# Kernel tuning notes

Measured on AMD Instinct MI355X. Metric: run time of the kernel, lower is better.

Reference implementation:

```python
import jax, jax.numpy as jnp
import numpy as np

B, N, C, H, L, M, V, NC = 8, 2048, 512, 8, 8, 128, 32000, 2
HD = C // H          # head dim = 64
HID = 4 * C          # MLP hidden = 2048
SCALE = HD ** -0.5
LN_EPS = 1e-5
FEAT_EPS = 1e-6


def _orth_matrix(d, m, rng):
    # gaussian_orthogonal_random_matrix: stack QR blocks of d x d
    blocks = []
    n_full, m_rem = divmod(m, d)
    for _ in range(n_full):
        Q, _ = np.linalg.qr(rng.standard_normal((d, d)))
        blocks.append(Q)
    if m_rem > 0:
        Q, _ = np.linalg.qr(rng.standard_normal((d, d)))
        blocks.append(Q[:, :m_rem])
    return np.concatenate(blocks, axis=1)


def setup_inputs() -> dict:
    key = jax.random.key(0)
    ks = jax.random.split(key, 32)
    rng = np.random.default_rng(0)

    def w(i, shape, s=0.02):
        return jax.random.normal(ks[i], shape, jnp.float32) * s

    proj = jnp.asarray(
        np.stack([np.stack([_orth_matrix(HD, M, rng) for _ in range(H)]) for _ in range(L)]),
        jnp.float32)  # [L, H, HD, M]

    inp = {
        "input_ids": jax.random.randint(ks[0], (B, N), 0, V),
        "attention_mask": jnp.ones((B, N), jnp.int32),
        "tok_emb": w(1, (V, C)),
        "cls": w(2, (1, 1, C)),
        "pos": w(3, (N + 1, C)),
        "ln1_g": jnp.ones((L, C), jnp.float32),
        "ln1_b": jnp.zeros((L, C), jnp.float32),
        "qW": w(4, (L, C, C)), "qb": jnp.zeros((L, C), jnp.float32),
        "kW": w(5, (L, C, C)), "kb": jnp.zeros((L, C), jnp.float32),
        "vW": w(6, (L, C, C)), "vb": jnp.zeros((L, C), jnp.float32),
        "oW": w(7, (L, C, C)), "ob": jnp.zeros((L, C), jnp.float32),
        "proj": proj,
        "ln2_g": jnp.ones((L, C), jnp.float32),
        "ln2_b": jnp.zeros((L, C), jnp.float32),
        "fc1W": w(8, (L, C, HID)), "fc1b": jnp.zeros((L, HID), jnp.float32),
        "fc2W": w(9, (L, HID, C)), "fc2b": jnp.zeros((L, C), jnp.float32),
        "lnf_g": jnp.ones((C,), jnp.float32),
        "lnf_b": jnp.zeros((C,), jnp.float32),
        "headW": w(10, (C, NC)),
        "headb": jnp.zeros((NC,), jnp.float32),
    }
    return inp


def _ln(x, g, b):
    mu = jnp.mean(x, axis=-1, keepdims=True)
    var = jnp.mean((x - mu) ** 2, axis=-1, keepdims=True)
    return (x - mu) * jax.lax.rsqrt(var + LN_EPS) * g + b


def _softmax_feature(x, p):
    # x: [B,Nt,H,HD], p: [H,HD,M]
    xw = jnp.einsum('bnhd,hdm->bnhm', x, p)
    x_sq = 0.5 * jnp.sum(x * x, axis=-1, keepdims=True)
    mx = jnp.max(xw, axis=-1, keepdims=True)
    return jnp.exp(xw - mx) * jnp.exp(mx - x_sq) + FEAT_EPS


def reference(input_ids, attention_mask, tok_emb, cls, pos, ln1_g, ln1_b,
              qW, qb, kW, kb, vW, vb, oW, ob, proj, ln2_g, ln2_b,
              fc1W, fc1b, fc2W, fc2b, lnf_g, lnf_b, headW, headb):
    x = tok_emb[input_ids]                                   # [B,N,C]
    x = jnp.concatenate([jnp.broadcast_to(cls, (B, 1, C)), x], axis=1)  # [B,Nt,C]
    x = x + pos[None]
    mask = jnp.concatenate(
        [jnp.ones((B, 1), x.dtype), attention_mask.astype(x.dtype)], axis=1)  # [B,Nt]
    mfeat = mask[:, :, None, None]

    Nt = N + 1
    for i in range(L):
        # Performer attention (FAVOR+)
        y = _ln(x, ln1_g[i], ln1_b[i])
        q = (y @ qW[i] + qb[i]).reshape(B, Nt, H, HD) * SCALE
        k = (y @ kW[i] + kb[i]).reshape(B, Nt, H, HD) * mfeat
        v = (y @ vW[i] + vb[i]).reshape(B, Nt, H, HD) * mfeat
        qf = _softmax_feature(q, proj[i])                    # [B,Nt,H,M]
        kf = _softmax_feature(k, proj[i])
        kv = jnp.einsum('bnhm,bnhd->bhmd', kf, v)            # [B,H,M,HD]
        ksum = jnp.sum(kf, axis=1)                           # [B,H,M]
        denom = jnp.maximum(jnp.einsum('bnhm,bhm->bhn', qf, ksum), 1e-6)[..., None]
        ctx = jnp.einsum('bnhm,bhmd->bhnd', qf, kv) / denom  # [B,H,Nt,HD]
        out = ctx.transpose(0, 2, 1, 3).reshape(B, Nt, C)
        x = x + (out @ oW[i] + ob[i])
        # MLP (exact GELU, as nn.GELU default)
        y = _ln(x, ln2_g[i], ln2_b[i])
        h = jax.nn.gelu(y @ fc1W[i] + fc1b[i], approximate=False)
        x = x + (h @ fc2W[i] + fc2b[i])

    x = _ln(x, lnf_g, lnf_b)
    return x[:, 0] @ headW + headb                           # [B,NC]
```

## Files before the change

### kernel.cpp

```cpp
#include <hip/hip_runtime.h>
#include <cmath>
#include <cstdint>
#include <cstddef>

#define B_ 8
#define N_ 2048
#define NT 2049
#define NP 2080
#define C_ 512
#define H_ 8
#define HD_ 64
#define L_ 8
#define M_ 128
#define HID_ 2048
#define NC_ 2
#define BNT (B_*NT)
#define RP (B_*NP)
#define SCALE_ 0.125f
#define LN_EPS_ 1e-5f
#define FEAT_EPS_ 1e-6f

#define MODE_GELU  2
#define MODE_RESID 3

typedef unsigned short u16;
typedef unsigned short u16x8 __attribute__((ext_vector_type(8)));
typedef short frag __attribute__((ext_vector_type(8)));
typedef float f32x4 __attribute__((ext_vector_type(4)));

constexpr size_t F_X    = 0;
constexpr size_t F_KVP  = F_X   + (size_t)RP*512;
constexpr size_t F_KSP  = F_KVP + (size_t)4*64*8192;
constexpr size_t F_KV   = F_KSP + (size_t)4*64*128;
constexpr size_t F_KS   = F_KV  + (size_t)64*M_*HD_;
constexpr size_t F_QKVB = F_KS  + (size_t)64*M_;
constexpr size_t F_END  = F_QKVB + 1536;
constexpr size_t S_BASE = 2 * F_END;
constexpr size_t S_Y    = S_BASE;
constexpr size_t S_V    = S_Y  + (size_t)RP*512;
constexpr size_t S_KF   = S_V  + (size_t)RP*512;
constexpr size_t S_QF   = S_KF + (size_t)RP*1024;
constexpr size_t S_WQKV = S_QF + (size_t)RP*1024;
constexpr size_t S_WO   = S_WQKV + (size_t)1536*512;
constexpr size_t S_WF1  = S_WO   + (size_t)512*512;
constexpr size_t S_WF2  = S_WF1  + (size_t)2048*512;
constexpr size_t S_PT   = S_WF2  + (size_t)512*2048;
constexpr size_t S_END  = S_PT   + (size_t)8*128*64;
constexpr size_t WS_BYTES = S_END * 2;

__device__ __forceinline__ float wave_reduce(float v) {
#pragma unroll
  for (int off = 32; off > 0; off >>= 1) v += __shfl_down(v, off, 64);
  return v;
}
__device__ __forceinline__ float b2f(u16 u) {
  union { float f; uint32_t i; } v; v.i = ((uint32_t)u) << 16; return v.f;
}
__device__ __forceinline__ u16 f2b(float f) {
  union { float f; uint32_t i; } v; v.f = f;
  uint32_t r = v.i + 0x7FFF + ((v.i >> 16) & 1);
  return (u16)(r >> 16);
}
__device__ __forceinline__ void gstage(const u16* g, u16* lds_base, int lane) {
#if __has_builtin(__builtin_amdgcn_global_load_lds)
  __builtin_amdgcn_global_load_lds((const __attribute__((address_space(1))) void*)g,
      (__attribute__((address_space(3))) void*)lds_base, 16, 0, 0);
#else
  *(u16x8*)(lds_base + lane * 8) = *(const u16x8*)g;
#endif
}
__device__ __forceinline__ void xcd_swz(int& bx, int& by) {
  int gx = gridDim.x;
  int nwg = gx * gridDim.y;
  int hw = blockIdx.x + blockIdx.y * gx;
  if (nwg & 7) { bx = blockIdx.x; by = blockIdx.y; return; }
  int cpx = nwg >> 3;
  int swz = (hw & 7) * cpx + (hw >> 3);
  bx = swz % gx; by = swz / gx;
}

__global__ __launch_bounds__(256) void embed_k(const int* __restrict__ ids,
    const float* __restrict__ tok, const float* __restrict__ cls,
    const float* __restrict__ pos, float* __restrict__ X) {
  int row = blockIdx.x;
  int b = row / NT, n = row - b * NT;
  int t = threadIdx.x;
  const float* src = (n == 0) ? cls : tok + (size_t)ids[b * N_ + n - 1] * C_;
  size_t rp = (size_t)b * NP + n;
  X[rp * C_ + t]       = src[t]       + pos[(size_t)n * C_ + t];
  X[rp * C_ + t + 256] = src[t + 256] + pos[(size_t)n * C_ + t + 256];
}

__global__ __launch_bounds__(256) void wconv_k(
    const float* __restrict__ qW, const float* __restrict__ kW,
    const float* __restrict__ vW, const float* __restrict__ oW,
    const float* __restrict__ f1W, const float* __restrict__ f2W,
    const float* __restrict__ projL,
    const float* __restrict__ qb, const float* __restrict__ kb,
    const float* __restrict__ vb,
    u16* __restrict__ Wqkv, u16* __restrict__ Wo,
    u16* __restrict__ Wf1, u16* __restrict__ Wf2,
    u16* __restrict__ PT, float* __restrict__ QKVB) {
  __shared__ float tile[32][33];
  int bid = blockIdx.x, t = threadIdx.x;
  if (bid >= 3104) {
    int i = (bid - 3104) * 256 + t;
    QKVB[i] = (i < 512) ? qb[i] : (i < 1024) ? kb[i - 512] : vb[i - 1024];
    return;
  }
  if (bid >= 3072) {
    int base = (bid - 3072) * 2048 + t * 8;
#pragma unroll
    for (int j = 0; j < 8; ++j) {
      int idx = base + j;
      int h = idx >> 13, rem = idx & 8191, m = rem >> 6, d = rem & 63;
      PT[idx] = f2b(projL[(size_t)h * 8192 + d * 128 + m]);
    }
    return;
  }
  int ti = t >> 5, tj = t & 31;
  const float* src; u16* dst; int k0, n0, ldn, ldk, scol;
  if (bid < 768) {
    int tk = bid & 15, tn = bid >> 4;
    k0 = tk * 32; n0 = tn * 32;
    int sel = n0 >> 9; scol = n0 & 511;
    src = (sel == 0) ? qW : (sel == 1) ? kW : vW;
    ldn = 512; dst = Wqkv; ldk = 512;
  } else if (bid < 1024) {
    int b2 = bid - 768;
    int tk = b2 & 15, tn = b2 >> 4;
    k0 = tk * 32; n0 = tn * 32; scol = n0;
    src = oW; ldn = 512; dst = Wo; ldk = 512;
  } else if (bid < 2048) {
    int b2 = bid - 1024;
    int tk = b2 & 15, tn = b2 >> 4;
    k0 = tk * 32; n0 = tn * 32; scol = n0;
    src = f1W; ldn = 2048; dst = Wf1; ldk = 512;
  } else {
    int b2 = bid - 2048;
    int tk = b2 & 63, tn = b2 >> 6;
    k0 = tk * 32; n0 = tn * 32; scol = n0;
    src = f2W; ldn = 512; dst = Wf2; ldk = 2048;
  }
  const float* sp = src + (size_t)k0 * ldn + scol;
  u16* dp = dst + (size_t)n0 * ldk + k0;
#pragma unroll
  for (int p = 0; p < 4; ++p)
    tile[ti + p * 8][tj] = sp[(size_t)(ti + p * 8) * ldn + tj];
  __syncthreads();
#pragma unroll
  for (int p = 0; p < 4; ++p)
    dp[(size_t)(ti + p * 8) * ldk + tj] = f2b(tile[tj][ti + p * 8]);
}

__global__ __launch_bounds__(256) void ln_bf_k(const float* __restrict__ X,
    const float* __restrict__ g, const float* __restrict__ b,
    u16* __restrict__ Y) {
  int w = threadIdx.x >> 6, lane = threadIdx.x & 63;
  int row = blockIdx.x * 4 + w;
  const float* xr = X + (size_t)row * C_;
  float v[8];
  *(float4*)&v[0] = *(const float4*)(xr + lane * 8);
  *(float4*)&v[4] = *(const float4*)(xr + lane * 8 + 4);
  float s = 0.f;
#pragma unroll
  for (int j = 0; j < 8; ++j) s += v[j];
  s = wave_reduce(s);
  float mu = __shfl(s, 0, 64) * (1.0f / C_);
  float sq = 0.f;
#pragma unroll
  for (int j = 0; j < 8; ++j) { float d = v[j] - mu; sq = fmaf(d, d, sq); }
  sq = wave_reduce(sq);
  float rs = rsqrtf(__shfl(sq, 0, 64) * (1.0f / C_) + LN_EPS_);
  float gv[8], bv[8];
  *(float4*)&gv[0] = *(const float4*)(g + lane * 8);
  *(float4*)&gv[4] = *(const float4*)(g + lane * 8 + 4);
  *(float4*)&bv[0] = *(const float4*)(b + lane * 8);
  *(float4*)&bv[4] = *(const float4*)(b + lane * 8 + 4);
  u16x8 o;
#pragma unroll
  for (int j = 0; j < 8; ++j) o[j] = f2b((v[j] - mu) * rs * gv[j] + bv[j]);
  *(u16x8*)(Y + (size_t)row * C_ + lane * 8) = o;
}

__global__ __launch_bounds__(256) void gemm_bf_k(
    const u16* __restrict__ A, int lda,
    const u16* __restrict__ Wt,
    const float* __restrict__ bias,
    float* __restrict__ outF, u16* __restrict__ outB,
    int ldc, int Kdim, int mode) {
  __shared__ __align__(16) u16 As[128 * 64];
  __shared__ __align__(16) u16 Bs[128 * 64];
  const int t = threadIdx.x, w = t >> 6, l = t & 63;
  int bx, by; xcd_swz(bx, by);
  const int row0 = by * 128, col0 = bx * 128;
  const int wm = w & 1, wn = w >> 1;
  const int lm = l & 15, lkb = l >> 4;
  const int lr = l >> 3, lc = l & 7;
  const int kch = (lc ^ lr) * 8;
  const u16* Ag = A  + (size_t)(row0 + lr) * lda  + kch;
  const u16* Bg = Wt + (size_t)(col0 + lr) * Kdim + kch;
  const int sx = lm & 7;
  f32x4 acc[4][4] = {};
  for (int k0 = 0; k0 < Kdim; k0 += 64) {
    __syncthreads();
#pragma unroll
    for (int j = 0; j < 4; ++j) {
      int c8 = w * 4 + j;
      gstage(Ag + (size_t)c8 * 8 * lda  + k0, &As[c8 * 512], l);
      gstage(Bg + (size_t)c8 * 8 * Kdim + k0, &Bs[c8 * 512], l);
    }
    __syncthreads();
#pragma unroll
    for (int ks = 0; ks < 2; ++ks) {
      frag af[4], bf4[4];
#pragma unroll
      for (int i = 0; i < 4; ++i)
        af[i] = *(const frag*)&As[(wm * 64 + i * 16 + lm) * 64 + (((ks * 4 + lkb) ^ sx) * 8)];
#pragma unroll
      for (int j = 0; j < 4; ++j)
        bf4[j] = *(const frag*)&Bs[(wn * 64 + j * 16 + lm) * 64 + (((ks * 4 + lkb) ^ sx) * 8)];
#pragma unroll
      for (int i = 0; i < 4; ++i)
#pragma unroll
        for (int j = 0; j < 4; ++j)
          acc[i][j] = __builtin_amdgcn_mfma_f32_16x16x32_bf16(af[i], bf4[j], acc[i][j], 0, 0, 0);
    }
  }
#pragma unroll
  for (int i = 0; i < 4; ++i) {
#pragma unroll
    for (int r = 0; r < 4; ++r) {
      int grow = row0 + wm * 64 + i * 16 + lkb * 4 + r;
      if (mode == MODE_RESID) {
        float* orow = outF + (size_t)grow * ldc + col0;
#pragma unroll
        for (int j = 0; j < 4; ++j) {
          int gc = wn * 64 + j * 16 + lm;
          orow[gc] += acc[i][j][r] + bias[col0 + gc];
        }
      } else {
        u16* orow = outB + (size_t)grow * ldc + col0;
#pragma unroll
        for (int j = 0; j < 4; ++j) {
          int gc = wn * 64 + j * 16 + lm;
          float v = acc[i][j][r] + bias[col0 + gc];
          float u = v * (1.5957691216f + 0.0713548162f * v * v);
          v = v / (1.f + __expf(-u));
          orow[gc] = f2b(v);
        }
      }
    }
  }
}

__global__ __launch_bounds__(256) void gemm_bf64_k(
    const u16* __restrict__ A, int lda,
    const u16* __restrict__ Wt,
    const float* __restrict__ bias,
    float* __restrict__ outF, u16* __restrict__ outB,
    int ldc, int Kdim, int mode) {
  __shared__ __align__(16) u16 As[64 * 64];
  __shared__ __align__(16) u16 Bs[128 * 64];
  const int t = threadIdx.x, w = t >> 6, l = t & 63;
  int bx, by; xcd_swz(bx, by);
  const int row0 = by * 64, col0 = bx * 128;
  const int wm = w & 1, wn = w >> 1;
  const int lm = l & 15, lkb = l >> 4;
  const int lr = l >> 3, lc = l & 7;
  const int kch = (lc ^ lr) * 8;
  const u16* Ag = A  + (size_t)(row0 + lr) * lda  + kch;
  const u16* Bg = Wt + (size_t)(col0 + lr) * Kdim + kch;
  const int sx = lm & 7;
  f32x4 acc[2][4] = {};
  for (int k0 = 0; k0 < Kdim; k0 += 64) {
    __syncthreads();
#pragma unroll
    for (int q = 0; q < 2; ++q) {
      int c8 = w * 2 + q;
      gstage(Ag + (size_t)c8 * 8 * lda + k0, &As[c8 * 512], l);
    }
#pragma unroll
    for (int q = 0; q < 4; ++q) {
      int c8 = w * 4 + q;
      gstage(Bg + (size_t)c8 * 8 * Kdim + k0, &Bs[c8 * 512], l);
    }
    __syncthreads();
#pragma unroll
    for (int ks = 0; ks < 2; ++ks) {
      frag af[2], bf4[4];
#pragma unroll
      for (int i = 0; i < 2; ++i)
        af[i] = *(const frag*)&As[(wm * 32 + i * 16 + lm) * 64 + (((ks * 4 + lkb) ^ sx) * 8)];
#pragma unroll
      for (int j = 0; j < 4; ++j)
        bf4[j] = *(const frag*)&Bs[(wn * 64 + j * 16 + lm) * 64 + (((ks * 4 + lkb) ^ sx) * 8)];
#pragma unroll
      for (int i = 0; i < 2; ++i)
#pragma unroll
        for (int j = 0; j < 4; ++j)
          acc[i][j] = __builtin_amdgcn_mfma_f32_16x16x32_bf16(af[i], bf4[j], acc[i][j], 0, 0, 0);
    }
  }
#pragma unroll
  for (int i = 0; i < 2; ++i) {
#pragma unroll
    for (int r = 0; r < 4; ++r) {
      int grow = row0 + wm * 32 + i * 16 + lkb * 4 + r;
      if (mode == MODE_RESID) {
        float* orow = outF + (size_t)grow * ldc + col0;
#pragma unroll
        for (int j = 0; j < 4; ++j) {
          int gc = wn * 64 + j * 16 + lm;
          orow[gc] += acc[i][j][r] + bias[col0 + gc];
        }
      } else {
        u16* orow = outB + (size_t)grow * ldc + col0;
#pragma unroll
        for (int j = 0; j < 4; ++j) {
          int gc = wn * 64 + j * 16 + lm;
          float v = acc[i][j][r] + bias[col0 + gc];
          float u = v * (1.5957691216f + 0.0713548162f * v * v);
          v = v / (1.f + __expf(-u));
          orow[gc] = f2b(v);
        }
      }
    }
  }
}

__global__ __launch_bounds__(256) void gemmqkv_k(
    const u16* __restrict__ A,
    const u16* __restrict__ Wt,
    const float* __restrict__ bias,
    u16* __restrict__ Vout,
    u16* __restrict__ QF, u16* __restrict__ KF,
    const u16* __restrict__ PT,
    const int* __restrict__ attn) {
  __shared__ __align__(16) u16 As[128 * 64];
  __shared__ __align__(16) u16 Bs[128 * 64];
  __shared__ __align__(16) u16 ptb[128 * 64];
  __shared__ float sxe[128][2];
  const int t = threadIdx.x, w = t >> 6, l = t & 63;
  int bx, by; xcd_swz(bx, by);
  const int cx = bx;
  const int row0 = by * 128, col0 = cx * 128;
  const int wm = w & 1, wn = w >> 1;
  const int lm = l & 15, lkb = l >> 4;
  const int lr = l >> 3, lc = l & 7;
  const int kch = (lc ^ lr) * 8;
  const u16* Ag = A  + (size_t)(row0 + lr) * 512 + kch;
  const u16* Bg = Wt + (size_t)(col0 + lr) * 512 + kch;
  const int sx = lm & 7;
  f32x4 acc[4][4] = {};
  for (int k0 = 0; k0 < 512; k0 += 64) {
    __syncthreads();
#pragma unroll
    for (int j = 0; j < 4; ++j) {
      int c8 = w * 4 + j;
      gstage(Ag + (size_t)c8 * 8 * 512 + k0, &As[c8 * 512], l);
      gstage(Bg + (size_t)c8 * 8 * 512 + k0, &Bs[c8 * 512], l);
    }
    __syncthreads();
#pragma unroll
    for (int ks = 0; ks < 2; ++ks) {
      frag af[4], bf4[4];
#pragma unroll
      for (int i = 0; i < 4; ++i)
        af[i] = *(const frag*)&As[(wm * 64 + i * 16 + lm) * 64 + (((ks * 4 + lkb) ^ sx) * 8)];
#pragma unroll
      for (int j = 0; j < 4; ++j)
        bf4[j] = *(const frag*)&Bs[(wn * 64 + j * 16 + lm) * 64 + (((ks * 4 + lkb) ^ sx) * 8)];
#pragma unroll
      for (int i = 0; i < 4; ++i)
#pragma unroll
        for (int j = 0; j < 4; ++j)
          acc[i][j] = __builtin_amdgcn_mfma_f32_16x16x32_bf16(af[i], bf4[j], acc[i][j], 0, 0, 0);
    }
  }
  if (cx >= 8) {
    int c0v = col0 - 1024;
#pragma unroll
    for (int i = 0; i < 4; ++i) {
#pragma unroll
      for (int r = 0; r < 4; ++r) {
        int grow = row0 + wm * 64 + i * 16 + lkb * 4 + r;
        int bb = grow / NP, nn = grow - bb * NP;
        float mrow = (nn == 0) ? 1.f : ((nn < NT) ? (float)attn[bb * N_ + nn - 1] : 0.f);
        u16* orow = Vout + (size_t)grow * 512 + c0v;
#pragma unroll
        for (int j = 0; j < 4; ++j) {
          int gc = wn * 64 + j * 16 + lm;
          orow[gc] = f2b((acc[i][j][r] + bias[col0 + gc]) * mrow);
        }
      }
    }
    return;
  }
  const bool isq = (cx < 4);
  const int hbase = (isq ? cx : cx - 4) * 2;
  __syncthreads();
  {
    u16* qt = wn ? Bs : As;
#pragma unroll
    for (int i = 0; i < 4; ++i) {
#pragma unroll
      for (int r = 0; r < 4; ++r) {
        int rl = wm * 64 + i * 16 + lkb * 4 + r;
        float mrow;
        if (isq) mrow = SCALE_;
        else {
          int grow = row0 + rl;
          int bb = grow / NP, nn = grow - bb * NP;
          mrow = (nn == 0) ? 1.f : ((nn < NT) ? (float)attn[bb * N_ + nn - 1] : 0.f);
        }
#pragma unroll
        for (int j = 0; j < 4; ++j) {
          int gcc = j * 16 + lm;
          float v = (acc[i][j][r] + bias[col0 + wn * 64 + gcc]) * mrow;
          qt[rl * 64 + (((gcc >> 3) ^ (rl & 7)) * 8) + (gcc & 7)] = f2b(v);
        }
      }
    }
  }
  {
    const u16* Pg = PT + (size_t)hbase * 8192 + (size_t)lr * 64 + kch;
#pragma unroll
    for (int q = 0; q < 4; ++q) {
      int c8 = w * 4 + q;
      gstage(Pg + (size_t)c8 * 8 * 64, &ptb[c8 * 512], l);
    }
  }
  __syncthreads();
  {
    int rowi = t >> 1, hf = t & 1;
    const u16* qq = hf ? Bs : As;
    float s = 0.f;
#pragma unroll
    for (int c = 0; c < 8; ++c) {
      const u16* p = &qq[rowi * 64 + ((c ^ (rowi & 7)) * 8)];
#pragma unroll
      for (int e = 0; e < 8; ++e) { float a = b2f(p[e]); s = fmaf(a, a, s); }
    }
    sxe[rowi][hf] = 0.5f * s;
  }
  __syncthreads();
  u16* OF = isq ? QF : KF;
#pragma unroll
  for (int hp = 0; hp < 2; ++hp) {
    if (hp == 1) {
      __syncthreads();
      const u16* Pg = PT + (size_t)(hbase + 1) * 8192 + (size_t)lr * 64 + kch;
#pragma unroll
      for (int q = 0; q < 4; ++q) {
        int c8 = w * 4 + q;
        gstage(Pg + (size_t)c8 * 8 * 64, &ptb[c8 * 512], l);
      }
      __syncthreads();
    }
    const u16* qt = hp ? Bs : As;
    f32x4 a2[2][8] = {};
#pragma unroll
    for (int ks = 0; ks < 2; ++ks) {
      frag af2[2], bf2[8];
#pragma unroll
      for (int i = 0; i < 2; ++i)
        af2[i] = *(const frag*)&qt[(w * 32 + i * 16 + lm) * 64 + (((ks * 4 + lkb) ^ sx) * 8)];
#pragma unroll
      for (int j = 0; j < 8; ++j)
        bf2[j] = *(const frag*)&ptb[(j * 16 + lm) * 64 + (((ks * 4 + lkb) ^ sx) * 8)];
#pragma unroll
      for (int i = 0; i < 2; ++i)
#pragma unroll
        for (int j = 0; j < 8; ++j)
          a2[i][j] = __builtin_amdgcn_mfma_f32_16x16x32_bf16(af2[i], bf2[j], a2[i][j], 0, 0, 0);
    }
    int hg = hbase + hp;
#pragma unroll
    for (int i = 0; i < 2; ++i) {
#pragma unroll
      for (int r = 0; r < 4; ++r) {
        int R = w * 32 + i * 16 + lkb * 4 + r;
        int grow = row0 + R;
        int bb = grow / NP, nn = grow - bb * NP;
        bool valid = nn < NT;
        float xs = sxe[R][hp];
        u16* orow = OF + (size_t)grow * 1024 + (size_t)hg * 128;
#pragma unroll
        for (int j = 0; j < 8; ++j) {
          int m = j * 16 + lm;
          float v = valid ? (__expf(a2[i][j][r] - xs) + FEAT_EPS_) : 0.f;
          orow[m] = f2b(v);
        }
      }
    }
  }
}

__global__ __launch_bounds__(256) void kvpart_k(const u16* __restrict__ KF,
    const u16* __restrict__ Vb, float* __restrict__ KVP,
    float* __restrict__ KSP) {
  int ci = blockIdx.x, bh = blockIdx.y;
  int b = bh >> 3, h = bh & 7;
  size_t rb0 = (size_t)b * NP + ci * 520;
  __shared__ __align__(16) float kfs[8 * 132];
  __shared__ __align__(16) float vsm[8 * 68];
  int t = threadIdx.x;
  const int d0 = (t & 7) * 8, m0 = (t >> 3) * 4;
  const bool hk = t < 128;
  const bool hv = (t >= 128) && (t < 192);
  const int ktok = t >> 4, kmj = (t & 15) * 8;
  const int vtok = (t - 128) >> 3, vdj = (t & 7) * 8;
  float acc[4][8] = {};
  float ks[4] = {};
  u16x8 rk, rv;
  if (hk) rk = *(const u16x8*)&KF[(rb0 + ktok) * 1024 + h * 128 + kmj];
  if (hv) rv = *(const u16x8*)&Vb[(rb0 + vtok) * 512 + h * 64 + vdj];
  for (int tile = 0; tile < 65; ++tile) {
    if (hk) {
#pragma unroll
      for (int e = 0; e < 8; ++e) kfs[ktok * 132 + kmj + e] = b2f(rk[e]);
    }
    if (hv) {
#pragma unroll
      for (int e = 0; e < 8; ++e) vsm[vtok * 68 + vdj + e] = b2f(rv[e]);
    }
    __syncthreads();
    if (tile + 1 < 65) {
      size_t rb = rb0 + (size_t)(tile + 1) * 8;
      if (hk) rk = *(const u16x8*)&KF[(rb + ktok) * 1024 + h * 128 + kmj];
      if (hv) rv = *(const u16x8*)&Vb[(rb + vtok) * 512 + h * 64 + vdj];
    }
#pragma unroll
    for (int tok = 0; tok < 8; ++tok) {
      float kq[4], va[8];
      *(float4*)&kq[0] = *(const float4*)&kfs[tok * 132 + m0];
      *(float4*)&va[0] = *(const float4*)&vsm[tok * 68 + d0];
      *(float4*)&va[4] = *(const float4*)&vsm[tok * 68 + d0 + 4];
#pragma unroll
      for (int mi = 0; mi < 4; ++mi)
#pragma unroll
        for (int di = 0; di < 8; ++di)
          acc[mi][di] = fmaf(kq[mi], va[di], acc[mi][di]);
      if ((t & 7) == 0) { ks[0] += kq[0]; ks[1] += kq[1]; ks[2] += kq[2]; ks[3] += kq[3]; }
    }
    __syncthreads();
  }
  size_t base = ((size_t)ci * 64 + bh) * 8192;
#pragma unroll
  for (int mi = 0; mi < 4; ++mi)
#pragma unroll
    for (int di = 0; di < 8; ++di)
      KVP[base + (size_t)(m0 + mi) * 64 + d0 + di] = acc[mi][di];
  if ((t & 7) == 0) {
#pragma unroll
    for (int mi = 0; mi < 4; ++mi)
      KSP[((size_t)ci * 64 + bh) * 128 + m0 + mi] = ks[mi];
  }
}

__global__ __launch_bounds__(256) void kvred_k(const float* __restrict__ KVP,
    const float* __restrict__ KSP, float* __restrict__ KV,
    float* __restrict__ KSUM) {
  int bh = blockIdx.x, t = threadIdx.x;
#pragma unroll
  for (int p = 0; p < 32; ++p) {
    int e = p * 256 + t;
    float s = 0.f;
#pragma unroll
    for (int ci = 0; ci < 4; ++ci) s += KVP[((size_t)ci * 64 + bh) * 8192 + e];
    KV[(size_t)bh * 8192 + e] = s;
  }
  if (t < 128) {
    float s = 0.f;
#pragma unroll
    for (int ci = 0; ci < 4; ++ci) s += KSP[((size_t)ci * 64 + bh) * 128 + t];
    KSUM[(size_t)bh * 128 + t] = s;
  }
}

__global__ __launch_bounds__(256) void ctx_k(const u16* __restrict__ QF,
    const float* __restrict__ KVg, const float* __restrict__ KSUM,
    u16* __restrict__ CTXo) {
  __shared__ float qfs[128 * 36];
  __shared__ float kvs[128 * 68];
  __shared__ float ksums[128];
  __shared__ float dls[32];
  __shared__ float dpart[8 * 32];
  int t = threadIdx.x;
  int bx, by; xcd_swz(bx, by);
  int bh = by; int b = bh >> 3, h = bh & 7;
  int n0 = bx * 32;
  size_t rbase = (size_t)b * NP + n0;
#pragma unroll
  for (int p = 0; p < 16; ++p) {
    int e = p * 256 + t; int m = e & 127; int tok = e >> 7;
    qfs[m * 36 + tok] = b2f(QF[(rbase + tok) * 1024 + h * 128 + m]);
  }
#pragma unroll
  for (int p = 0; p < 32; ++p) {
    int e = p * 256 + t;
    kvs[(e >> 6) * 68 + (e & 63)] = KVg[(size_t)bh * 8192 + e];
  }
  if (t < 128) ksums[t] = KSUM[bh * 128 + t];
  __syncthreads();
  {
    int j = t & 31, pp = t >> 5;
    float s = 0.f;
#pragma unroll
    for (int mi = 0; mi < 16; ++mi) {
      int m = pp * 16 + mi;
      s = fmaf(qfs[m * 36 + j], ksums[m], s);
    }
    dpart[pp * 32 + j] = s;
  }
  __syncthreads();
  if (t < 32) {
    float den = 0.f;
#pragma unroll
    for (int pp = 0; pp < 8; ++pp) den += dpart[pp * 32 + t];
    dls[t] = 1.f / fmaxf(den, 1e-6f);
  }
  __syncthreads();
  {
    const int d0 = (t & 15) * 4, tok0 = (t >> 4) * 2;
    float acc[2][4] = {};
#pragma unroll 16
    for (int m = 0; m < 128; ++m) {
      float q0 = qfs[m * 36 + tok0];
      float q1 = qfs[m * 36 + tok0 + 1];
      float4 kv4 = *(const float4*)&kvs[m * 68 + d0];
      acc[0][0] = fmaf(q0, kv4.x, acc[0][0]); acc[0][1] = fmaf(q0, kv4.y, acc[0][1]);
      acc[0][2] = fmaf(q0, kv4.z, acc[0][2]); acc[0][3] = fmaf(q0, kv4.w, acc[0][3]);
      acc[1][0] = fmaf(q1, kv4.x, acc[1][0]); acc[1][1] = fmaf(q1, kv4.y, acc[1][1]);
      acc[1][2] = fmaf(q1, kv4.z, acc[1][2]); acc[1][3] = fmaf(q1, kv4.w, acc[1][3]);
    }
#pragma unroll
    for (int r = 0; r < 2; ++r) {
      int n = n0 + tok0 + r;
      if (n >= NT) continue;
      float rd = dls[tok0 + r];
      u16* o = CTXo + (rbase + tok0 + r) * C_ + h * HD_ + d0;
#pragma unroll
      for (int c = 0; c < 4; ++c) o[c] = f2b(acc[r][c] * rd);
    }
  }
}

__global__ __launch_bounds__(256) void final_k(const float* __restrict__ X,
    const float* __restrict__ g, const float* __restrict__ beta,
    const float* __restrict__ hW, const float* __restrict__ hb,
    float* __restrict__ out) {
  int b = blockIdx.x, t = threadIdx.x;
  const float* xr = X + (size_t)b * NP * C_;
  float v0 = xr[t], v1 = xr[t + 256];
  __shared__ float red[4][4];
  float s = wave_reduce(v0 + v1);
  if ((t & 63) == 0) red[0][t >> 6] = s;
  __syncthreads();
  float mu = (red[0][0] + red[0][1] + red[0][2] + red[0][3]) * (1.0f / C_);
  float d0 = v0 - mu, d1 = v1 - mu;
  float s2 = wave_reduce(d0 * d0 + d1 * d1);
  if ((t & 63) == 0) red[1][t >> 6] = s2;
  __syncthreads();
  float var = (red[1][0] + red[1][1] + red[1][2] + red[1][3]) * (1.0f / C_);
  float rs = rsqrtf(var + LN_EPS_);
  float n0 = d0 * rs * g[t] + beta[t];
  float n1 = d1 * rs * g[t + 256] + beta[t + 256];
  float p0 = n0 * hW[t * NC_]     + n1 * hW[(t + 256) * NC_];
  float p1 = n0 * hW[t * NC_ + 1] + n1 * hW[(t + 256) * NC_ + 1];
  float t0 = wave_reduce(p0);
  float t1 = wave_reduce(p1);
  if ((t & 63) == 0) { red[2][t >> 6] = t0; red[3][t >> 6] = t1; }
  __syncthreads();
  if (t == 0) {
    out[b * NC_]     = red[2][0] + red[2][1] + red[2][2] + red[2][3] + hb[0];
    out[b * NC_ + 1] = red[3][0] + red[3][1] + red[3][2] + red[3][3] + hb[1];
  }
}

extern "C" void kernel_launch(void* const* d_in, const int* in_sizes, int n_in,
                              void* d_out, int out_size, void* d_ws, size_t ws_size,
                              hipStream_t stream) {
  if (ws_size < WS_BYTES) return;
  const int*   ids   = (const int*)d_in[0];
  const int*   attn  = (const int*)d_in[1];
  const float* tok   = (const float*)d_in[2];
  const float* cls   = (const float*)d_in[3];
  const float* pos   = (const float*)d_in[4];
  const float* ln1g  = (const float*)d_in[5];
  const float* ln1b  = (const float*)d_in[6];
  const float* qW    = (const float*)d_in[7];
  const float* qb    = (const float*)d_in[8];
  const float* kW    = (const float*)d_in[9];
  const float* kb    = (const float*)d_in[10];
  const float* vW    = (const float*)d_in[11];
  const float* vb    = (const float*)d_in[12];
  const float* oW    = (const float*)d_in[13];
  const float* ob    = (const float*)d_in[14];
  const float* proj  = (const float*)d_in[15];
  const float* ln2g  = (const float*)d_in[16];
  const float* ln2b  = (const float*)d_in[17];
  const float* fc1W  = (const float*)d_in[18];
  const float* fc1b  = (const float*)d_in[19];
  const float* fc2W  = (const float*)d_in[20];
  const float* fc2b  = (const float*)d_in[21];
  const float* lnfg  = (const float*)d_in[22];
  const float* lnfb  = (const float*)d_in[23];
  const float* headW = (const float*)d_in[24];
  const float* headb = (const float*)d_in[25];

  float* ws  = (float*)d_ws;
  u16*   wsu = (u16*)d_ws;
  float* X    = ws + F_X;
  float* KVP  = ws + F_KVP;
  float* KSP  = ws + F_KSP;
  float* KV   = ws + F_KV;
  float* KSUM = ws + F_KS;
  float* QKVB = ws + F_QKVB;
  u16* Ybf  = wsu + S_Y;
  u16* CTXb = wsu + S_Y;
  u16* Vb   = wsu + S_V;
  u16* HB   = wsu + S_V;
  u16* KFb  = wsu + S_KF;
  u16* QFb  = wsu + S_QF;
  u16* Wqkv = wsu + S_WQKV;
  u16* Wo   = wsu + S_WO;
  u16* Wf1  = wsu + S_WF1;
  u16* Wf2  = wsu + S_WF2;
  u16* PT   = wsu + S_PT;

  embed_k<<<BNT, 256, 0, stream>>>(ids, tok, cls, pos, X);
  for (int i = 0; i < L_; ++i) {
    wconv_k<<<3110, 256, 0, stream>>>(qW + (size_t)i * C_ * C_, kW + (size_t)i * C_ * C_,
        vW + (size_t)i * C_ * C_, oW + (size_t)i * C_ * C_,
        fc1W + (size_t)i * C_ * HID_, fc2W + (size_t)i * HID_ * C_,
        proj + (size_t)i * H_ * HD_ * M_,
        qb + i * C_, kb + i * C_, vb + i * C_,
        Wqkv, Wo, Wf1, Wf2, PT, QKVB);
    ln_bf_k<<<RP / 4, 256, 0, stream>>>(X, ln1g + i * C_, ln1b + i * C_, Ybf);
    gemmqkv_k<<<dim3(12, 130), 256, 0, stream>>>(Ybf, Wqkv, QKVB,
        Vb, QFb, KFb, PT, attn);
    kvpart_k<<<dim3(4, 64), 256, 0, stream>>>(KFb, Vb, KVP, KSP);
    kvred_k<<<64, 256, 0, stream>>>(KVP, KSP, KV, KSUM);
    ctx_k<<<dim3(65, 64), 256, 0, stream>>>(QFb, KV, KSUM, CTXb);
    gemm_bf64_k<<<dim3(4, 260), 256, 0, stream>>>(CTXb, 512, Wo, ob + i * C_,
        X, nullptr, 512, 512, MODE_RESID);
    ln_bf_k<<<RP / 4, 256, 0, stream>>>(X, ln2g + i * C_, ln2b + i * C_, Ybf);
    gemm_bf_k<<<dim3(16, 130), 256, 0, stream>>>(Ybf, 512, Wf1,
        fc1b + i * HID_, nullptr, HB, 2048, 512, MODE_GELU);
    gemm_bf64_k<<<dim3(4, 260), 256, 0, stream>>>(HB, 2048, Wf2,
        fc2b + i * C_, X, nullptr, 512, 2048, MODE_RESID);
  }
  final_k<<<B_, 256, 0, stream>>>(X, lnfg, lnfb, headW, headb, (float*)d_out);
}
```

Measured before the change: 3.193 ms.

## Double-buffer LDS tiles in bf16 GEMM kernels to overlap loads with MFMA

Both GEMM kernels now keep two LDS buffers for A and B tiles. The next k-tile is issued with direct global-to-LDS staging before computing the current one, and explicit vmcnt waits plus raw barriers replace the per-iteration __syncthreads pair. This is meant to hide global load latency behind the MFMA work. In exchange LDS use doubles, to 64KB per block for the 128x128 kernel, which can lower occupancy, and correctness now depends on the hand-counted vmcnt values matching the number of staging loads.

```diff
diff --git a/kernel.cpp b/kernel.cpp
--- a/kernel.cpp
+++ b/kernel.cpp
@@ -189,8 +189,8 @@
     const float* __restrict__ bias,
     float* __restrict__ outF, u16* __restrict__ outB,
     int ldc, int Kdim, int mode) {
-  __shared__ __align__(16) u16 As[128 * 64];
-  __shared__ __align__(16) u16 Bs[128 * 64];
+  __shared__ __align__(16) u16 As[2][128 * 64];
+  __shared__ __align__(16) u16 Bs[2][128 * 64];
   const int t = threadIdx.x, w = t >> 6, l = t & 63;
   int bx, by; xcd_swz(bx, by);
   const int row0 = by * 128, col0 = bx * 128;
@@ -202,30 +202,46 @@
   const u16* Bg = Wt + (size_t)(col0 + lr) * Kdim + kch;
   const int sx = lm & 7;
   f32x4 acc[4][4] = {};
-  for (int k0 = 0; k0 < Kdim; k0 += 64) {
-    __syncthreads();
-#pragma unroll
-    for (int j = 0; j < 4; ++j) {
-      int c8 = w * 4 + j;
-      gstage(Ag + (size_t)c8 * 8 * lda  + k0, &As[c8 * 512], l);
-      gstage(Bg + (size_t)c8 * 8 * Kdim + k0, &Bs[c8 * 512], l);
-    }
-    __syncthreads();
+  const int nk = Kdim >> 6;
+#pragma unroll
+  for (int j = 0; j < 4; ++j) {
+    int c8 = w * 4 + j;
+    gstage(Ag + (size_t)c8 * 8 * lda , &As[0][c8 * 512], l);
+    gstage(Bg + (size_t)c8 * 8 * Kdim, &Bs[0][c8 * 512], l);
+  }
+  for (int kt = 0; kt < nk; ++kt) {
+    const int cur = kt & 1;
+    if (kt + 1 < nk) {
+      const int k0 = (kt + 1) << 6;
+#pragma unroll
+      for (int j = 0; j < 4; ++j) {
+        int c8 = w * 4 + j;
+        gstage(Ag + (size_t)c8 * 8 * lda  + k0, &As[cur ^ 1][c8 * 512], l);
+        gstage(Bg + (size_t)c8 * 8 * Kdim + k0, &Bs[cur ^ 1][c8 * 512], l);
+      }
+      asm volatile("s_waitcnt vmcnt(8)" ::: "memory");
+    } else {
+      asm volatile("s_waitcnt vmcnt(0)" ::: "memory");
+    }
+    __builtin_amdgcn_s_barrier();
+    __builtin_amdgcn_sched_barrier(0);
 #pragma unroll
     for (int ks = 0; ks < 2; ++ks) {
       frag af[4], bf4[4];
 #pragma unroll
       for (int i = 0; i < 4; ++i)
-        af[i] = *(const frag*)&As[(wm * 64 + i * 16 + lm) * 64 + (((ks * 4 + lkb) ^ sx) * 8)];
+        af[i] = *(const frag*)&As[cur][(wm * 64 + i * 16 + lm) * 64 + (((ks * 4 + lkb) ^ sx) * 8)];
 #pragma unroll
       for (int j = 0; j < 4; ++j)
-        bf4[j] = *(const frag*)&Bs[(wn * 64 + j * 16 + lm) * 64 + (((ks * 4 + lkb) ^ sx) * 8)];
+        bf4[j] = *(const frag*)&Bs[cur][(wn * 64 + j * 16 + lm) * 64 + (((ks * 4 + lkb) ^ sx) * 8)];
 #pragma unroll
       for (int i = 0; i < 4; ++i)
 #pragma unroll
         for (int j = 0; j < 4; ++j)
           acc[i][j] = __builtin_amdgcn_mfma_f32_16x16x32_bf16(af[i], bf4[j], acc[i][j], 0, 0, 0);
     }
+    __builtin_amdgcn_sched_barrier(0);
+    __builtin_amdgcn_s_barrier();
   }
 #pragma unroll
   for (int i = 0; i < 4; ++i) {
@@ -260,8 +276,8 @@
     const float* __restrict__ bias,
     float* __restrict__ outF, u16* __restrict__ outB,
     int ldc, int Kdim, int mode) {
-  __shared__ __align__(16) u16 As[64 * 64];
-  __shared__ __align__(16) u16 Bs[128 * 64];
+  __shared__ __align__(16) u16 As[2][64 * 64];
+  __shared__ __align__(16) u16 Bs[2][128 * 64];
   const int t = threadIdx.x, w = t >> 6, l = t & 63;
   int bx, by; xcd_swz(bx, by);
   const int row0 = by * 64, col0 = bx * 128;
@@ -273,34 +289,54 @@
   const u16* Bg = Wt + (size_t)(col0 + lr) * Kdim + kch;
   const int sx = lm & 7;
   f32x4 acc[2][4] = {};
-  for (int k0 = 0; k0 < Kdim; k0 += 64) {
-    __syncthreads();
-#pragma unroll
-    for (int q = 0; q < 2; ++q) {
-      int c8 = w * 2 + q;
-      gstage(Ag + (size_t)c8 * 8 * lda + k0, &As[c8 * 512], l);
-    }
-#pragma unroll
-    for (int q = 0; q < 4; ++q) {
-      int c8 = w * 4 + q;
-      gstage(Bg + (size_t)c8 * 8 * Kdim + k0, &Bs[c8 * 512], l);
-    }
-    __syncthreads();
+  const int nk = Kdim >> 6;
+#pragma unroll
+  for (int q = 0; q < 2; ++q) {
+    int c8 = w * 2 + q;
+    gstage(Ag + (size_t)c8 * 8 * lda, &As[0][c8 * 512], l);
+  }
+#pragma unroll
+  for (int q = 0; q < 4; ++q) {
+    int c8 = w * 4 + q;
+    gstage(Bg + (size_t)c8 * 8 * Kdim, &Bs[0][c8 * 512], l);
+  }
+  for (int kt = 0; kt < nk; ++kt) {
+    const int cur = kt & 1;
+    if (kt + 1 < nk) {
+      const int k0 = (kt + 1) << 6;
+#pragma unroll
+      for (int q = 0; q < 2; ++q) {
+        int c8 = w * 2 + q;
+        gstage(Ag + (size_t)c8 * 8 * lda + k0, &As[cur ^ 1][c8 * 512], l);
+      }
+#pragma unroll
+      for (int q = 0; q < 4; ++q) {
+        int c8 = w * 4 + q;
+        gstage(Bg + (size_t)c8 * 8 * Kdim + k0, &Bs[cur ^ 1][c8 * 512], l);
+      }
+      asm volatile("s_waitcnt vmcnt(6)" ::: "memory");
+    } else {
+      asm volatile("s_waitcnt vmcnt(0)" ::: "memory");
+    }
+    __builtin_amdgcn_s_barrier();
+    __builtin_amdgcn_sched_barrier(0);
 #pragma unroll
     for (int ks = 0; ks < 2; ++ks) {
       frag af[2], bf4[4];
 #pragma unroll
       for (int i = 0; i < 2; ++i)
-        af[i] = *(const frag*)&As[(wm * 32 + i * 16 + lm) * 64 + (((ks * 4 + lkb) ^ sx) * 8)];
+        af[i] = *(const frag*)&As[cur][(wm * 32 + i * 16 + lm) * 64 + (((ks * 4 + lkb) ^ sx) * 8)];
 #pragma unroll
       for (int j = 0; j < 4; ++j)
-        bf4[j] = *(const frag*)&Bs[(wn * 64 + j * 16 + lm) * 64 + (((ks * 4 + lkb) ^ sx) * 8)];
+        bf4[j] = *(const frag*)&Bs[cur][(wn * 64 + j * 16 + lm) * 64 + (((ks * 4 + lkb) ^ sx) * 8)];
 #pragma unroll
       for (int i = 0; i < 2; ++i)
 #pragma unroll
         for (int j = 0; j < 4; ++j)
           acc[i][j] = __builtin_amdgcn_mfma_f32_16x16x32_bf16(af[i], bf4[j], acc[i][j], 0, 0, 0);
     }
+    __builtin_amdgcn_sched_barrier(0);
+    __builtin_amdgcn_s_barrier();
   }
 #pragma unroll
   for (int i = 0; i < 2; ++i) {
```

Result: faster. 3.117 ms (-2.4%).
